# Kernel optimization log

Hardware: AMD Instinct MI355X
Metric: run time of the kernel (lower is better)

The kernel has to match this reference:

```python
import jax, jax.numpy as jnp
import numpy as np

BINS = 256
EPS = 1e-8


def _norm255(x):
    # (x - min) / (max - min) * 255, truncated to int (torch .int())
    mx = jnp.max(x, axis=(2, 3), keepdims=True)
    mn = jnp.min(x, axis=(2, 3), keepdims=True)
    return ((x - mn) / (mx - mn) * 255.0).astype(jnp.int32)


def _hist256(x):
    # x int32 [B,C,H,W] -> per-(b,c) 256-bin histogram [B,C,256] float32
    B, C = x.shape[0], x.shape[1]
    flat = x.reshape(B * C, -1)
    rows = jnp.arange(B * C)[:, None]
    h = jnp.zeros((B * C, BINS), jnp.float32).at[rows, flat].add(1.0)
    return h.reshape(B, C, BINS)


def _entropy(x):
    # faithful to Entropy(): p = hist / (H*W); h = -sum p*log(p+1e-8)
    B, C, H, W = x.shape
    p = _hist256(x) / (H * W)
    h = -jnp.sum(p * jnp.log(p + EPS), axis=2)
    return h[:, :, None, None]  # [B,C,1,1]


def _joint_entropy(x_p, x_ms):
    # Faithful to Joint_entropy's quirky count: for each (i,j) it counts pixels
    # where (x_ms==i AND x_p==j) OR (x_ms!=i AND x_p!=j).
    # count[i,j] = 2*J[i,j] + npix - hist_ms[i] - hist_p[j], J = joint histogram.
    B, C, H, W = x_ms.shape
    npix = H * W
    bins = jnp.arange(BINS)
    M = (x_ms.reshape(B, C, npix)[..., None] == bins).astype(jnp.float32)  # [B,C,P,256]
    P = (x_p.reshape(B, npix)[..., None] == bins).astype(jnp.float32)      # [B,P,256]
    J = jnp.einsum('bcpi,bpj->bcij', M, P)                                  # [B,C,256,256]
    hist_ms = jnp.sum(M, axis=2)  # [B,C,256]
    hist_p = jnp.sum(P, axis=1)   # [B,256]
    count = 2.0 * J + npix - hist_ms[:, :, :, None] - hist_p[:, None, None, :]
    p = count / float(BINS * BINS)  # original divides by 256*256, not npix
    h = -jnp.sum(p * jnp.log(p + EPS), axis=(2, 3))
    return h[:, :, None, None]  # [B,C,1,1]


def _channel(f_p, f_ms):
    B, C, H, W = f_p.shape
    f_p_m = jnp.mean(f_p, axis=1, keepdims=True)  # [B,1,H,W]
    # AdaptiveAvgPool2d((16,16)) with H,W divisible by 16 == block mean
    pooled = f_p.reshape(B, C, 16, H // 16, 16, W // 16).mean(axis=(3, 5))
    f_p_a = jnp.mean(pooled, axis=1, keepdims=True)  # [B,1,16,16]
    f_ms_n = _norm255(f_ms)
    f_p_m_n = _norm255(f_p_m)
    f_p_a_n = _norm255(f_p_a)
    h_ms = _entropy(f_ms_n)                 # [B,C,1,1]
    h_p = _entropy(f_p_m_n)                 # [B,1,1,1]
    h_ms_p = _joint_entropy(f_p_a_n, f_ms_n)  # [B,C,1,1]
    mi = h_p + h_ms - h_ms_p
    mi = jax.nn.softmax(mi, axis=1)  # nn.Softmax() on 4D -> dim=1
    return f_ms + f_ms * mi


def _similarity(f_p, f_ms):
    B, C, H, W = f_p.shape
    f_ms_u = jax.image.resize(f_ms, (B, C, H, W), method='bilinear')
    a = f_ms_u.reshape(B, C, -1)
    b = f_p.reshape(B, C, -1)
    a = a - jnp.mean(a, axis=2, keepdims=True)
    b = b - jnp.mean(b, axis=2, keepdims=True)
    na = jnp.sqrt(jnp.sum(a * a, axis=2))  # [B,C] (ms norms)
    nb = jnp.sqrt(jnp.sum(b * b, axis=2))  # [B,C] (p norms)
    s = jnp.einsum('bcp,bdp->bcd', a, b)   # [B,C,C]
    return s / ((na * nb) / 100.0)[:, :, None]


def _spatial(f_p, f_ms):
    B, C, H, W = f_p.shape
    s_m = _similarity(f_p, f_ms)
    mx = jnp.max(s_m, axis=2)        # [B,C]
    idx = jnp.argmax(s_m, axis=2)    # [B,C] best f_p channel per ms channel
    scores = jax.nn.softmax(mx, axis=1)
    brow = jnp.arange(B)[:, None]
    # group score: sum of softmax scores of ms-channels that picked value v
    g = jnp.zeros((B, C), scores.dtype).at[brow, idx].add(scores)
    cnt = jnp.zeros((B, C), jnp.int32).at[brow, idx].add(1)
    k = jnp.min(jnp.sum(cnt > 0, axis=1))  # min #unique over batch
    min_k = (k + 1) // 2                   # ceil(min_k / 2)
    order = jnp.argsort(-g, axis=1)        # descending group score; absent groups (0) sort last
    sorted_scores = jnp.take_along_axis(g, order, axis=1)  # [B,C]
    pos_mask = jnp.arange(C) < min_k       # keep top min_k positions
    z = jnp.where(pos_mask[None, :], sorted_scores, -jnp.inf)
    w = jax.nn.softmax(z, axis=1)          # softmax over selected scores, 0 elsewhere
    gathered = jnp.take_along_axis(f_p, order[:, :, None, None], axis=1)  # [B,C,H,W]
    mask = jnp.sum(w[:, :, None, None] * jax.nn.sigmoid(gathered), axis=1, keepdims=True)
    return f_p + f_p * mask


def setup_inputs() -> dict:
    key = jax.random.key(0)
    k1, k2 = jax.random.split(key)
    f_p = jax.random.normal(k1, (8, 64, 256, 256), dtype=jnp.float32)
    f_ms = jax.random.normal(k2, (8, 64, 16, 16), dtype=jnp.float32)
    return {"f_p": f_p, "f_ms": f_ms}


def reference(f_p, f_ms):
    rel_ms = _channel(f_p, f_ms)
    rel_p = _spatial(f_p, f_ms)
    return (rel_p, rel_ms)
```

## Files before the change

### kernel.cpp

```cpp
#include <hip/hip_runtime.h>

#define BB 8
#define CC 64
#define HP 256
#define WP 256
#define PP 65536
#define QQ 256

__device__ __forceinline__ unsigned encF(float f) {
    unsigned u = __float_as_uint(f);
    return (u & 0x80000000u) ? ~u : (u | 0x80000000u);
}
__device__ __forceinline__ float decF(unsigned u) {
    unsigned b = (u & 0x80000000u) ? (u ^ 0x80000000u) : ~u;
    return __uint_as_float(b);
}

__device__ __forceinline__ double blockSumD(double v, double* red4) {
    int t = threadIdx.x;
    for (int d = 32; d; d >>= 1) v += __shfl_down(v, d, 64);
    __syncthreads();
    if ((t & 63) == 0) red4[t >> 6] = v;
    __syncthreads();
    double r = red4[0] + red4[1] + red4[2] + red4[3];
    __syncthreads();
    return r;
}

__global__ __launch_bounds__(256) void k34_fused(const float* __restrict__ fp,
                                                 const float* __restrict__ fms,
                                                 float* __restrict__ cellsum,
                                                 float* __restrict__ gtent,
                                                 double* __restrict__ chsumD,
                                                 double* __restrict__ chsumsqD,
                                                 int* __restrict__ msn,
                                                 int* __restrict__ histms,
                                                 float* __restrict__ hmsE,
                                                 float* __restrict__ naArr,
                                                 float* __restrict__ mssum) {
    int blk = blockIdx.x;
    if (blk < 2048) {
        int qg = blk & 3, c = (blk >> 2) & 63, b = blk >> 8;
        int x = threadIdx.x, s = x >> 4, r = x & 15;
        const float* src = fp + (size_t)(b * CC + c) * PP;
        __shared__ float tentL[256];
        __shared__ double red4[4];
        tentL[x] = 0.0f;
        __syncthreads();
        float wm, w0, wp;
        if (x <= 7)        { wm = 0.f; w0 = 1.f; wp = 0.f; }
        else if (x >= 248) { wm = 0.f; w0 = 1.f; wp = 0.f; }
        else if (r < 8)    { float fx = ((float)r + 8.5f) * 0.0625f; wm = 1.f - fx; w0 = fx;       wp = 0.f; }
        else               { float fx = ((float)r - 7.5f) * 0.0625f; wm = 0.f;      w0 = 1.f - fx; wp = fx;  }
        double sum = 0.0, ssq = 0.0;
        for (int qi = 0; qi < 4; ++qi) {
            int q = qg * 4 + qi;
            float am = 0.f, a0 = 0.f, ap = 0.f, cs = 0.f;
#pragma unroll
            for (int ry = 0; ry < 16; ++ry) {
                float v = src[(q * 16 + ry) * 256 + x];
                sum += (double)v;
                ssq += (double)v * (double)v;
                cs  += v;
                if ((q == 0 && ry < 8) || (q == 15 && ry >= 8)) {
                    a0 += v;
                } else if (ry < 8) {
                    float fy = ((float)ry + 8.5f) * 0.0625f;
                    am += (1.f - fy) * v; a0 += fy * v;
                } else {
                    float fy = ((float)ry - 7.5f) * 0.0625f;
                    a0 += (1.f - fy) * v; ap += fy * v;
                }
            }
            float vals[10];
            vals[0] = am * wm; vals[1] = am * w0; vals[2] = am * wp;
            vals[3] = a0 * wm; vals[4] = a0 * w0; vals[5] = a0 * wp;
            vals[6] = ap * wm; vals[7] = ap * w0; vals[8] = ap * wp;
            vals[9] = cs;
#pragma unroll
            for (int d = 8; d; d >>= 1) {
#pragma unroll
                for (int k2 = 0; k2 < 10; ++k2) vals[k2] += __shfl_down(vals[k2], d, 16);
            }
            if (r == 0) {
                if (q > 0) {
                    if (s > 0)  atomicAdd(&tentL[(q - 1) * 16 + (s - 1)], vals[0]);
                    atomicAdd(&tentL[(q - 1) * 16 + s], vals[1]);
                    if (s < 15) atomicAdd(&tentL[(q - 1) * 16 + (s + 1)], vals[2]);
                }
                if (s > 0)  atomicAdd(&tentL[q * 16 + (s - 1)], vals[3]);
                atomicAdd(&tentL[q * 16 + s], vals[4]);
                if (s < 15) atomicAdd(&tentL[q * 16 + (s + 1)], vals[5]);
                if (q < 15) {
                    if (s > 0)  atomicAdd(&tentL[(q + 1) * 16 + (s - 1)], vals[6]);
                    atomicAdd(&tentL[(q + 1) * 16 + s], vals[7]);
                    if (s < 15) atomicAdd(&tentL[(q + 1) * 16 + (s + 1)], vals[8]);
                }
                cellsum[(size_t)(b * CC + c) * QQ + q * 16 + s] = vals[9];
            }
        }
        __syncthreads();
        int row = x >> 4;
        int rlo = qg * 4 - 1; if (rlo < 0) rlo = 0;
        int rhi = qg * 4 + 4; if (rhi > 15) rhi = 15;
        if (row >= rlo && row <= rhi) {
            atomicAdd(&gtent[(size_t)(b * CC + c) * QQ + x], tentL[x]);
        }
        double st = blockSumD(sum, red4);
        double sq = blockSumD(ssq, red4);
        if (x == 0) {
            atomicAdd(&chsumD[b * CC + c], st);
            atomicAdd(&chsumsqD[b * CC + c], sq);
        }
    } else {
        int blk2 = blk - 2048, b = blk2 >> 6, c = blk2 & 63, t = threadIdx.x;
        __shared__ float m[256];
        __shared__ int hist[256];
        __shared__ double red4[4];
        __shared__ double U[256];
        __shared__ unsigned umn, umx;
        float v = fms[(size_t)(b * CC + c) * QQ + t];
        m[t] = v;
        hist[t] = 0;
        if (t == 0) { umn = 0xFFFFFFFFu; umx = 0u; }
        float mn = v, mx = v;
        for (int d = 32; d; d >>= 1) {
            mn = fminf(mn, __shfl_down(mn, d, 64));
            mx = fmaxf(mx, __shfl_down(mx, d, 64));
        }
        __syncthreads();
        if ((t & 63) == 0) { atomicMin(&umn, encF(mn)); atomicMax(&umx, encF(mx)); }
        __syncthreads();
        mn = decF(umn); mx = decF(umx);
        int bin = (int)((v - mn) / (mx - mn) * 255.0f);
        bin = min(max(bin, 0), 255);
        msn[(size_t)(b * CC + c) * QQ + t] = bin;
        atomicAdd(&hist[bin], 1);
        __syncthreads();
        histms[(size_t)(b * CC + c) * QQ + t] = hist[t];
        float pf = (float)hist[t] * (1.0f / 256.0f);
        double term = -(double)(pf * __logf(pf + 1e-8f));
        double h = blockSumD(term, red4);
        if (t == 0) hmsE[b * CC + c] = (float)h;
        int i = t >> 4, j = t & 15;
        double kdj = (j == 0 || j == 15) ? 13.328125 : 10.65625;
        double mv = (double)m[t];
        double uu = kdj * mv + 2.671875 * ((j > 0 ? (double)m[t - 1] : 0.0) +
                                           (j < 15 ? (double)m[t + 1] : 0.0));
        U[t] = uu;
        __syncthreads();
        double kdi = (i == 0 || i == 15) ? 13.328125 : 10.65625;
        double vv = kdi * U[t] + 2.671875 * ((i > 0 ? U[t - 16] : 0.0) +
                                             (i < 15 ? U[t + 16] : 0.0));
        double sq = blockSumD(mv * vv, red4);
        double msm = blockSumD(mv, red4);
        if (t == 0) {
            mssum[b * CC + c] = (float)msm;
            double meanu = msm * (1.0 / 256.0);
            double na2 = sq - 65536.0 * meanu * meanu;
            naArr[b * CC + c] = (float)sqrt(na2 > 0.0 ? na2 : 0.0);
        }
    }
}

__global__ __launch_bounds__(256) void kC5_pa(const float* __restrict__ cellsum,
                                              int* __restrict__ pan,
                                              int* __restrict__ histp) {
    int b = blockIdx.x, t = threadIdx.x;
    __shared__ int hist[256];
    __shared__ unsigned umn, umx;
    hist[t] = 0;
    if (t == 0) { umn = 0xFFFFFFFFu; umx = 0u; }
    double acc = 0.0;
    for (int c = 0; c < CC; ++c) acc += (double)cellsum[(size_t)(b * CC + c) * QQ + t];
    float pa = (float)(acc * (1.0 / 256.0) * (1.0 / 64.0));
    float mn2 = pa, mx2 = pa;
    for (int d = 32; d; d >>= 1) {
        mn2 = fminf(mn2, __shfl_down(mn2, d, 64));
        mx2 = fmaxf(mx2, __shfl_down(mx2, d, 64));
    }
    __syncthreads();
    if ((t & 63) == 0) { atomicMin(&umn, encF(mn2)); atomicMax(&umx, encF(mx2)); }
    __syncthreads();
    mn2 = decF(umn); mx2 = decF(umx);
    int bin = (int)((pa - mn2) / (mx2 - mn2) * 255.0f);
    bin = min(max(bin, 0), 255);
    pan[b * QQ + t] = bin;
    atomicAdd(&hist[bin], 1);
    __syncthreads();
    histp[b * 256 + t] = hist[t];
}

__global__ __launch_bounds__(256) void k86_fused(const float* __restrict__ fms,
                                                 const float* __restrict__ gtent,
                                                 const float* __restrict__ mssum,
                                                 const double* __restrict__ chsumD,
                                                 const double* __restrict__ chsumsqD,
                                                 const float* __restrict__ naArr,
                                                 const int* __restrict__ msn,
                                                 const int* __restrict__ pan,
                                                 const int* __restrict__ histms,
                                                 const int* __restrict__ histp,
                                                 float* __restrict__ mxArr,
                                                 int* __restrict__ idxArr,
                                                 float* __restrict__ hjoint) {
    int blk0 = blockIdx.x;
    if (blk0 < 512) {
        int blk = blk0, b = blk >> 6, c = blk & 63, t = threadIdx.x;
        __shared__ float msrow[256];
        __shared__ double part[256];
        __shared__ double sval[64];
        msrow[t] = fms[(size_t)(b * CC + c) * QQ + t];
        __syncthreads();
        int d = t >> 2, pr = t & 3;
        const float* g = gtent + (size_t)(b * CC + d) * QQ + pr * 64;
        const float* mr = msrow + pr * 64;
        double acc = 0.0;
        for (int q2 = 0; q2 < 64; ++q2) acc += (double)mr[q2] * (double)g[q2];
        part[t] = acc;
        __syncthreads();
        if (t < 64) {
            double meanu = (double)mssum[b * CC + c] * (1.0 / 256.0);
            double meanp = chsumD[b * CC + t] * (1.0 / 65536.0);
            sval[t] = part[t * 4] + part[t * 4 + 1] + part[t * 4 + 2] + part[t * 4 + 3]
                      - 65536.0 * meanu * meanp;
        }
        __syncthreads();
        if (t == 0) {
            double best = sval[0]; int bi2 = 0;
            for (int dd = 1; dd < 64; ++dd) { if (sval[dd] > best) { best = sval[dd]; bi2 = dd; } }
            double nac = (double)naArr[b * CC + c];
            double sc_ = chsumD[b * CC + c];
            double sq_ = chsumsqD[b * CC + c];
            double nb2 = sq_ - sc_ * sc_ * (1.0 / 65536.0);
            double nbc = sqrt(nb2 > 0.0 ? nb2 : 0.0);
            mxArr[b * CC + c] = (float)(best * 100.0 / (nac * nbc));
            idxArr[b * CC + c] = bi2;
        }
    } else {
        int blk = blk0 - 512, b = blk >> 6, c = blk & 63, t = threadIdx.x;
        __shared__ int key[256], hms[256], hp[256];
        __shared__ double red4[4];
        int iv = msn[(size_t)(b * CC + c) * QQ + t];
        int jv = pan[b * QQ + t];
        key[t] = (iv << 8) | jv;
        hms[t] = histms[(size_t)(b * CC + c) * QQ + t];
        hp[t] = histp[b * 256 + t];
        __syncthreads();
        unsigned long long w0_ = 0, w1_ = 0, w2_ = 0, w3_ = 0;
        for (int p = 0; p < 256; ++p) {
            int k2 = key[p];
            if ((k2 >> 8) == t) {
                int j = k2 & 255;
                unsigned long long bit = 1ull << (j & 63);
                int w = j >> 6;
                if (w == 0) w0_ |= bit; else if (w == 1) w1_ |= bit;
                else if (w == 2) w2_ |= bit; else w3_ |= bit;
            }
        }
        double acc = 0.0;
        int basei = 256 - hms[t];
        unsigned long long words[4] = { w0_, w1_, w2_, w3_ };
#pragma unroll
        for (int w = 0; w < 4; ++w) {
            unsigned long long word = words[w];
            for (int jj = 0; jj < 64; ++jj) {
                if (!((word >> jj) & 1ull)) {
                    int cnt = basei - hp[w * 64 + jj];
                    float pf = (float)cnt * (1.0f / 65536.0f);
                    acc -= (double)(pf * __logf(pf + 1e-8f));
                }
            }
        }
        int myk = key[t], n = 0; bool first = true;
        for (int p = 0; p < 256; ++p) {
            int k2 = key[p];
            if (k2 == myk) { n++; if (p < t) first = false; }
        }
        if (first) {
            int cnt = 2 * n + 256 - hms[myk >> 8] - hp[myk & 255];
            float pf = (float)cnt * (1.0f / 65536.0f);
            acc -= (double)(pf * __logf(pf + 1e-8f));
        }
        double h = blockSumD(acc, red4);
        if (t == 0) hjoint[b * CC + c] = (float)h;
    }
}

__global__ __launch_bounds__(512) void k9_small(const float* __restrict__ mxArr,
                                                const int* __restrict__ idxArr,
                                                float* __restrict__ wsel,
                                                int* __restrict__ chanA,
                                                int* __restrict__ minkA) {
    __shared__ double sc[8][64];
    __shared__ double gs[8][64];
    __shared__ int idxS[8][64];
    __shared__ int ordv[8][64];
    __shared__ int uarr[8];
    __shared__ int mkS;
    int t = threadIdx.x;
    int b = t >> 6, c = t & 63;
    double v = (double)mxArr[b * 64 + c];
    double mx = v;
    for (int d = 32; d; d >>= 1) mx = fmax(mx, __shfl_down(mx, d, 64));
    mx = __shfl(mx, 0, 64);
    double e = exp(v - mx);
    double s = e;
    for (int d = 32; d; d >>= 1) s += __shfl_down(s, d, 64);
    s = __shfl(s, 0, 64);
    sc[b][c] = e / s;
    idxS[b][c] = idxArr[b * 64 + c];
    __syncthreads();
    double g = 0.0; int cnt = 0;
    for (int c2 = 0; c2 < 64; ++c2) {
        if (idxS[b][c2] == c) { g += sc[b][c2]; cnt++; }
    }
    gs[b][c] = g;
    unsigned long long ball = __ballot(cnt > 0);
    if (c == 0) uarr[b] = __popcll(ball);
    __syncthreads();
    if (t == 0) {
        int k = uarr[0];
        for (int b2 = 1; b2 < 8; ++b2) k = min(k, uarr[b2]);
        mkS = (k + 1) >> 1;
        minkA[0] = mkS;
    }
    __syncthreads();
    int rk = 0;
    double myg = gs[b][c];
    for (int c3 = 0; c3 < 64; ++c3) {
        double a = gs[b][c3];
        if (a > myg || (a == myg && c3 < c)) rk++;
    }
    ordv[b][rk] = c;
    __syncthreads();
    int mk = mkS;
    double z0 = gs[b][ordv[b][0]];
    double ee = (c < mk) ? exp(gs[b][ordv[b][c]] - z0) : 0.0;
    double se = ee;
    for (int d = 32; d; d >>= 1) se += __shfl_down(se, d, 64);
    se = __shfl(se, 0, 64);
    if (c < mk) {
        wsel[b * 64 + c] = (float)(ee / se);
        chanA[b * 64 + c] = ordv[b][c];
    }
}

__global__ __launch_bounds__(256) void kM_mask(const float* __restrict__ fp,
                                               const float* __restrict__ wsel,
                                               const int* __restrict__ chanA,
                                               const int* __restrict__ minkA,
                                               float* __restrict__ maskB) {
    int b = blockIdx.y;
    int i4 = blockIdx.x * 256 + threadIdx.x;
    int mk = minkA[0];
    const float4* src = (const float4*)(fp + (size_t)b * CC * PP);
    float mx0 = 0.f, mx1 = 0.f, mx2 = 0.f, mx3 = 0.f;
    for (int i = 0; i < mk; ++i) {
        int ch = chanA[b * 64 + i];
        float wv = wsel[b * 64 + i];
        float4 v = src[(size_t)ch * (PP / 4) + i4];
        mx0 += wv * (1.0f / (1.0f + __expf(-v.x)));
        mx1 += wv * (1.0f / (1.0f + __expf(-v.y)));
        mx2 += wv * (1.0f / (1.0f + __expf(-v.z)));
        mx3 += wv * (1.0f / (1.0f + __expf(-v.w)));
    }
    ((float4*)(maskB + (size_t)b * PP))[i4] = make_float4(mx0, mx1, mx2, mx3);
}

__global__ __launch_bounds__(256) void k10_relp(const float* __restrict__ fp,
                                                const float* __restrict__ maskB,
                                                float* __restrict__ outp,
                                                float* __restrict__ fpm,
                                                unsigned* __restrict__ minmax) {
    int b = blockIdx.y;
    int i4 = blockIdx.x * 256 + threadIdx.x;
    const float4* src = (const float4*)(fp + (size_t)b * CC * PP);
    float4 mk4 = ((const float4*)(maskB + (size_t)b * PP))[i4];
    float sx = 0.f, sy = 0.f, sz = 0.f, sw = 0.f;
    float4* dst = (float4*)(outp + (size_t)b * CC * PP);
    for (int c2 = 0; c2 < CC; ++c2) {
        float4 v = src[(size_t)c2 * (PP / 4) + i4];
        sx += v.x; sy += v.y; sz += v.z; sw += v.w;
        float4 o;
        o.x = v.x + v.x * mk4.x;
        o.y = v.y + v.y * mk4.y;
        o.z = v.z + v.z * mk4.z;
        o.w = v.w + v.w * mk4.w;
        dst[(size_t)c2 * (PP / 4) + i4] = o;
    }
    const float inv = 1.0f / 64.0f;
    float4 m; m.x = sx * inv; m.y = sy * inv; m.z = sz * inv; m.w = sw * inv;
    ((float4*)(fpm + (size_t)b * PP))[i4] = m;
    float mn = fminf(fminf(m.x, m.y), fminf(m.z, m.w));
    float mxv = fmaxf(fmaxf(m.x, m.y), fmaxf(m.z, m.w));
    for (int d = 32; d; d >>= 1) {
        mn = fminf(mn, __shfl_down(mn, d, 64));
        mxv = fmaxf(mxv, __shfl_down(mxv, d, 64));
    }
    __shared__ unsigned smn, smx;
    if (threadIdx.x == 0) { smn = 0u; smx = 0u; }
    __syncthreads();
    if ((threadIdx.x & 63) == 0) { atomicMax(&smn, ~encF(mn)); atomicMax(&smx, encF(mxv)); }
    __syncthreads();
    if (threadIdx.x == 0) { atomicMax(&minmax[2 * b], smn); atomicMax(&minmax[2 * b + 1], smx); }
}

__global__ __launch_bounds__(256) void k2a_hist(const float* __restrict__ fpm,
                                                const unsigned* __restrict__ minmax,
                                                int* __restrict__ histpm) {
    int b = blockIdx.y;
    __shared__ int h[256];
    h[threadIdx.x] = 0;
    __syncthreads();
    float mn = decF(~minmax[2 * b]);
    float mx = decF(minmax[2 * b + 1]);
    float dd = mx - mn;
    int i4 = blockIdx.x * 256 + threadIdx.x;
    float4 v = ((const float4*)(fpm + (size_t)b * PP))[i4];
    int b0 = (int)((v.x - mn) / dd * 255.0f);
    int b1 = (int)((v.y - mn) / dd * 255.0f);
    int b2 = (int)((v.z - mn) / dd * 255.0f);
    int b3 = (int)((v.w - mn) / dd * 255.0f);
    b0 = min(max(b0, 0), 255); b1 = min(max(b1, 0), 255);
    b2 = min(max(b2, 0), 255); b3 = min(max(b3, 0), 255);
    atomicAdd(&h[b0], 1); atomicAdd(&h[b1], 1);
    atomicAdd(&h[b2], 1); atomicAdd(&h[b3], 1);
    __syncthreads();
    atomicAdd(&histpm[b * 256 + threadIdx.x], h[threadIdx.x]);
}

__global__ __launch_bounds__(256) void kF_relms(const int* __restrict__ histpm,
                                                const float* __restrict__ fms,
                                                const float* __restrict__ hmsE,
                                                const float* __restrict__ hjoint,
                                                float* __restrict__ out2) {
    int b = blockIdx.x, t = threadIdx.x;
    __shared__ double red4[4];
    __shared__ double mi[64];
    __shared__ float hpEs;
    int n = histpm[b * 256 + t];
    float p = (float)n * (1.0f / 65536.0f);
    double term = -(double)(p * __logf(p + 1e-8f));
    double h = blockSumD(term, red4);
    if (t == 0) hpEs = (float)h;
    __syncthreads();
    if (t < 64) mi[t] = (double)hpEs + (double)hmsE[b * CC + t] - (double)hjoint[b * CC + t];
    __syncthreads();
    if (t == 0) {
        double mxv = mi[0];
        for (int c2 = 1; c2 < 64; ++c2) if (mi[c2] > mxv) mxv = mi[c2];
        double s = 0.0;
        for (int c2 = 0; c2 < 64; ++c2) { mi[c2] = exp(mi[c2] - mxv); s += mi[c2]; }
        for (int c2 = 0; c2 < 64; ++c2) mi[c2] /= s;
    }
    __syncthreads();
    const float* srcm = fms + (size_t)b * CC * QQ;
    float* dstm = out2 + (size_t)b * CC * QQ;
    for (int e = t; e < CC * QQ; e += 256) {
        float v = srcm[e];
        float miv = (float)mi[e >> 8];
        dstm[e] = v + v * miv;
    }
}

extern "C" void kernel_launch(void* const* d_in, const int* in_sizes, int n_in,
                              void* d_out, int out_size, void* d_ws, size_t ws_size,
                              hipStream_t stream) {
    const float* fp = (const float*)d_in[0];
    const float* fms = (const float*)d_in[1];
    float* out = (float*)d_out;

    char* p = (char*)d_ws;
    auto alloc = [&](size_t bytes) { void* r = (void*)p; p += (bytes + 255) & ~(size_t)255; return r; };

    float* fpm      = (float*)alloc((size_t)BB * PP * 4);
    float* maskB    = (float*)alloc((size_t)BB * PP * 4);
    float* cellsum  = (float*)alloc((size_t)BB * CC * QQ * 4);
    char* zbeg = p;
    float* gtent    = (float*)alloc((size_t)BB * CC * QQ * 4);
    double* chsumD  = (double*)alloc((size_t)BB * CC * 8);
    double* chsumsqD= (double*)alloc((size_t)BB * CC * 8);
    unsigned* minmax= (unsigned*)alloc((size_t)BB * 2 * 4);
    int* histpm     = (int*)alloc((size_t)BB * 256 * 4);
    size_t zlen = (size_t)(p - zbeg);
    int* msn        = (int*)alloc((size_t)BB * CC * QQ * 4);
    int* histms     = (int*)alloc((size_t)BB * CC * 256 * 4);
    int* histp      = (int*)alloc((size_t)BB * 256 * 4);
    int* pan        = (int*)alloc((size_t)BB * QQ * 4);
    float* hmsE     = (float*)alloc((size_t)BB * CC * 4);
    float* hjoint   = (float*)alloc((size_t)BB * CC * 4);
    float* naArr    = (float*)alloc((size_t)BB * CC * 4);
    float* mssum    = (float*)alloc((size_t)BB * CC * 4);
    float* mxArr    = (float*)alloc((size_t)BB * CC * 4);
    int* idxArr     = (int*)alloc((size_t)BB * CC * 4);
    float* wsel     = (float*)alloc((size_t)BB * CC * 4);
    int* chanA      = (int*)alloc((size_t)BB * CC * 4);
    int* minkA      = (int*)alloc(256);

    float* out_relp  = out;
    float* out_relms = out + (size_t)BB * CC * PP;

    hipMemsetAsync(zbeg, 0, zlen, stream);
    k34_fused<<<2560, 256, 0, stream>>>(fp, fms, cellsum, gtent, chsumD, chsumsqD,
                                        msn, histms, hmsE, naArr, mssum);
    kC5_pa<<<8, 256, 0, stream>>>(cellsum, pan, histp);
    k86_fused<<<1024, 256, 0, stream>>>(fms, gtent, mssum, chsumD, chsumsqD, naArr,
                                        msn, pan, histms, histp, mxArr, idxArr, hjoint);
    k9_small<<<1, 512, 0, stream>>>(mxArr, idxArr, wsel, chanA, minkA);
    kM_mask<<<dim3(64, 8), 256, 0, stream>>>(fp, wsel, chanA, minkA, maskB);
    k10_relp<<<dim3(64, 8), 256, 0, stream>>>(fp, maskB, out_relp, fpm, minmax);
    k2a_hist<<<dim3(64, 8), 256, 0, stream>>>(fpm, minmax, histpm);
    kF_relms<<<8, 256, 0, stream>>>(histpm, fms, hmsE, hjoint, out_relms);
}
```

Baseline: 398.8 us.

## Fuse mask into relp kernel, split stats blocks finer, accumulate pooled sums atomically

Merges the sigmoid-weighted mask computation into the output kernel, so the mask is no longer written to and re-read from global memory. The statistics kernel now gives each block 2 cell rows instead of 4, doubling the number of blocks. The per-channel cell sums are no longer stored and re-summed over 64 channels later; they are accumulated into a per-batch double buffer with atomics. The trade-off is more double-precision atomics, more blocks, and one kernel that has to hold the mask in registers while it loops over channels.

Measured after the change: 383.8 us (median of 2 runs). 3.7% less time.

```diff
diff --git a/kernel.cpp b/kernel.cpp
--- a/kernel.cpp
+++ b/kernel.cpp
@@ -29,7 +29,7 @@
 
 __global__ __launch_bounds__(256) void k34_fused(const float* __restrict__ fp,
                                                  const float* __restrict__ fms,
-                                                 float* __restrict__ cellsum,
+                                                 double* __restrict__ pasumD,
                                                  float* __restrict__ gtent,
                                                  double* __restrict__ chsumD,
                                                  double* __restrict__ chsumsqD,
@@ -39,8 +39,8 @@
                                                  float* __restrict__ naArr,
                                                  float* __restrict__ mssum) {
     int blk = blockIdx.x;
-    if (blk < 2048) {
-        int qg = blk & 3, c = (blk >> 2) & 63, b = blk >> 8;
+    if (blk < 4096) {
+        int qg = blk & 7, c = (blk >> 3) & 63, b = blk >> 9;
         int x = threadIdx.x, s = x >> 4, r = x & 15;
         const float* src = fp + (size_t)(b * CC + c) * PP;
         __shared__ float tentL[256];
@@ -53,8 +53,9 @@
         else if (r < 8)    { float fx = ((float)r + 8.5f) * 0.0625f; wm = 1.f - fx; w0 = fx;       wp = 0.f; }
         else               { float fx = ((float)r - 7.5f) * 0.0625f; wm = 0.f;      w0 = 1.f - fx; wp = fx;  }
         double sum = 0.0, ssq = 0.0;
-        for (int qi = 0; qi < 4; ++qi) {
-            int q = qg * 4 + qi;
+#pragma unroll
+        for (int qi = 0; qi < 2; ++qi) {
+            int q = qg * 2 + qi;
             float am = 0.f, a0 = 0.f, ap = 0.f, cs = 0.f;
 #pragma unroll
             for (int ry = 0; ry < 16; ++ry) {
@@ -96,13 +97,13 @@
                     atomicAdd(&tentL[(q + 1) * 16 + s], vals[7]);
                     if (s < 15) atomicAdd(&tentL[(q + 1) * 16 + (s + 1)], vals[8]);
                 }
-                cellsum[(size_t)(b * CC + c) * QQ + q * 16 + s] = vals[9];
+                atomicAdd(&pasumD[b * 256 + q * 16 + s], (double)vals[9]);
             }
         }
         __syncthreads();
         int row = x >> 4;
-        int rlo = qg * 4 - 1; if (rlo < 0) rlo = 0;
-        int rhi = qg * 4 + 4; if (rhi > 15) rhi = 15;
+        int rlo = qg * 2 - 1; if (rlo < 0) rlo = 0;
+        int rhi = qg * 2 + 2; if (rhi > 15) rhi = 15;
         if (row >= rlo && row <= rhi) {
             atomicAdd(&gtent[(size_t)(b * CC + c) * QQ + x], tentL[x]);
         }
@@ -113,7 +114,7 @@
             atomicAdd(&chsumsqD[b * CC + c], sq);
         }
     } else {
-        int blk2 = blk - 2048, b = blk2 >> 6, c = blk2 & 63, t = threadIdx.x;
+        int blk2 = blk - 4096, b = blk2 >> 6, c = blk2 & 63, t = threadIdx.x;
         __shared__ float m[256];
         __shared__ int hist[256];
         __shared__ double red4[4];
@@ -163,7 +164,7 @@
     }
 }
 
-__global__ __launch_bounds__(256) void kC5_pa(const float* __restrict__ cellsum,
+__global__ __launch_bounds__(256) void kC5_pa(const double* __restrict__ pasumD,
                                               int* __restrict__ pan,
                                               int* __restrict__ histp) {
     int b = blockIdx.x, t = threadIdx.x;
@@ -171,8 +172,7 @@
     __shared__ unsigned umn, umx;
     hist[t] = 0;
     if (t == 0) { umn = 0xFFFFFFFFu; umx = 0u; }
-    double acc = 0.0;
-    for (int c = 0; c < CC; ++c) acc += (double)cellsum[(size_t)(b * CC + c) * QQ + t];
+    double acc = pasumD[b * 256 + t];
     float pa = (float)(acc * (1.0 / 256.0) * (1.0 / 64.0));
     float mn2 = pa, mx2 = pa;
     for (int d = 32; d; d >>= 1) {
@@ -346,11 +346,13 @@
     }
 }
 
-__global__ __launch_bounds__(256) void kM_mask(const float* __restrict__ fp,
-                                               const float* __restrict__ wsel,
-                                               const int* __restrict__ chanA,
-                                               const int* __restrict__ minkA,
-                                               float* __restrict__ maskB) {
+__global__ __launch_bounds__(256) void k10_relp(const float* __restrict__ fp,
+                                                const float* __restrict__ wsel,
+                                                const int* __restrict__ chanA,
+                                                const int* __restrict__ minkA,
+                                                float* __restrict__ outp,
+                                                float* __restrict__ fpm,
+                                                unsigned* __restrict__ minmax) {
     int b = blockIdx.y;
     int i4 = blockIdx.x * 256 + threadIdx.x;
     int mk = minkA[0];
@@ -365,28 +367,16 @@
         mx2 += wv * (1.0f / (1.0f + __expf(-v.z)));
         mx3 += wv * (1.0f / (1.0f + __expf(-v.w)));
     }
-    ((float4*)(maskB + (size_t)b * PP))[i4] = make_float4(mx0, mx1, mx2, mx3);
-}
-
-__global__ __launch_bounds__(256) void k10_relp(const float* __restrict__ fp,
-                                                const float* __restrict__ maskB,
-                                                float* __restrict__ outp,
-                                                float* __restrict__ fpm,
-                                                unsigned* __restrict__ minmax) {
-    int b = blockIdx.y;
-    int i4 = blockIdx.x * 256 + threadIdx.x;
-    const float4* src = (const float4*)(fp + (size_t)b * CC * PP);
-    float4 mk4 = ((const float4*)(maskB + (size_t)b * PP))[i4];
     float sx = 0.f, sy = 0.f, sz = 0.f, sw = 0.f;
     float4* dst = (float4*)(outp + (size_t)b * CC * PP);
     for (int c2 = 0; c2 < CC; ++c2) {
         float4 v = src[(size_t)c2 * (PP / 4) + i4];
         sx += v.x; sy += v.y; sz += v.z; sw += v.w;
         float4 o;
-        o.x = v.x + v.x * mk4.x;
-        o.y = v.y + v.y * mk4.y;
-        o.z = v.z + v.z * mk4.z;
-        o.w = v.w + v.w * mk4.w;
+        o.x = v.x + v.x * mx0;
+        o.y = v.y + v.y * mx1;
+        o.z = v.z + v.z * mx2;
+        o.w = v.w + v.w * mx3;
         dst[(size_t)c2 * (PP / 4) + i4] = o;
     }
     const float inv = 1.0f / 64.0f;
@@ -475,10 +465,9 @@
     auto alloc = [&](size_t bytes) { void* r = (void*)p; p += (bytes + 255) & ~(size_t)255; return r; };
 
     float* fpm      = (float*)alloc((size_t)BB * PP * 4);
-    float* maskB    = (float*)alloc((size_t)BB * PP * 4);
-    float* cellsum  = (float*)alloc((size_t)BB * CC * QQ * 4);
     char* zbeg = p;
     float* gtent    = (float*)alloc((size_t)BB * CC * QQ * 4);
+    double* pasumD  = (double*)alloc((size_t)BB * 256 * 8);
     double* chsumD  = (double*)alloc((size_t)BB * CC * 8);
     double* chsumsqD= (double*)alloc((size_t)BB * CC * 8);
     unsigned* minmax= (unsigned*)alloc((size_t)BB * 2 * 4);
@@ -502,14 +491,13 @@
     float* out_relms = out + (size_t)BB * CC * PP;
 
     hipMemsetAsync(zbeg, 0, zlen, stream);
-    k34_fused<<<2560, 256, 0, stream>>>(fp, fms, cellsum, gtent, chsumD, chsumsqD,
+    k34_fused<<<4608, 256, 0, stream>>>(fp, fms, pasumD, gtent, chsumD, chsumsqD,
                                         msn, histms, hmsE, naArr, mssum);
-    kC5_pa<<<8, 256, 0, stream>>>(cellsum, pan, histp);
+    kC5_pa<<<8, 256, 0, stream>>>(pasumD, pan, histp);
     k86_fused<<<1024, 256, 0, stream>>>(fms, gtent, mssum, chsumD, chsumsqD, naArr,
                                         msn, pan, histms, histp, mxArr, idxArr, hjoint);
     k9_small<<<1, 512, 0, stream>>>(mxArr, idxArr, wsel, chanA, minkA);
-    kM_mask<<<dim3(64, 8), 256, 0, stream>>>(fp, wsel, chanA, minkA, maskB);
-    k10_relp<<<dim3(64, 8), 256, 0, stream>>>(fp, maskB, out_relp, fpm, minmax);
+    k10_relp<<<dim3(64, 8), 256, 0, stream>>>(fp, wsel, chanA, minkA, out_relp, fpm, minmax);
     k2a_hist<<<dim3(64, 8), 256, 0, stream>>>(fpm, minmax, histpm);
     kF_relms<<<8, 256, 0, stream>>>(histpm, fms, hmsE, hjoint, out_relms);
 }
```
